# Kernel optimization log

Measured on AMD Instinct MI355X. Metric: run time of the kernel, lower is better.

## Reference

```python
import jax, jax.numpy as jnp
import numpy as np

EPS = 1e-7       # torchvision generalized_box_iou_loss eps
IMG_SIZE = 320.0  # labels are divided by 320 in the original criterion
NO_OBJ = 80       # class id 80 == no-object sentinel


def _hungarian(cost):
    """Jonker-Volgenant style shortest-augmenting-path LSA (== scipy.optimize.linear_sum_assignment).
    cost: [n, m] numpy array, n <= m. Returns (row_ind, col_ind) sorted by row."""
    cost = np.asarray(cost, dtype=np.float64)
    n, m = cost.shape
    INF = float("inf")
    u = np.zeros(n + 1)
    v = np.zeros(m + 1)
    p = np.zeros(m + 1, dtype=np.int64)   # p[j]: 1-based row matched to column j, 0 = free
    way = np.zeros(m + 1, dtype=np.int64)
    for i in range(1, n + 1):
        p[0] = i
        j0 = 0
        minv = np.full(m + 1, INF)
        used = np.zeros(m + 1, dtype=bool)
        while True:
            used[j0] = True
            i0 = p[j0]
            free = ~used[1:]
            cur = cost[i0 - 1] - u[i0] - v[1:]
            better = free & (cur < minv[1:])
            minv[1:] = np.where(better, cur, minv[1:])
            way[1:] = np.where(better, j0, way[1:])
            masked = np.where(free, minv[1:], INF)
            j1 = int(np.argmin(masked)) + 1
            delta = masked[j1 - 1]
            uj = np.nonzero(used)[0]
            u[p[uj]] += delta
            v[uj] -= delta
            minv[1:] = np.where(free, minv[1:] - delta, minv[1:])
            j0 = j1
            if p[j0] == 0:
                break
        while j0 != 0:
            j1 = way[j0]
            p[j0] = p[j1]
            j0 = j1
    cols = np.nonzero(p[1:])[0]
    rows = p[1:][cols] - 1
    order = np.argsort(rows)
    return rows[order], cols[order]


def _box_cxcywh_to_xyxy(b):
    cx, cy, w, h = b[..., 0], b[..., 1], b[..., 2], b[..., 3]
    return jnp.stack([cx - 0.5 * w, cy - 0.5 * h, cx + 0.5 * w, cy + 0.5 * h], axis=-1)


def _cost_matrix(prob_class, predict_bbox, labels):
    """Vectorized version of the original nested double loop: [B, n_pred, n_true] cost."""
    B, P, C = prob_class.shape
    T = labels.shape[1]
    lab_bbox = labels[..., :4] / IMG_SIZE          # [B,T,4] cxcywh in [0,1]
    cls = labels[..., 4].astype(jnp.int32)          # [B,T]

    # class NLL: -log p[b, pred, cls[b, true]]
    logp = jnp.log(prob_class)                      # [B,P,C]
    idx = jnp.broadcast_to(cls[:, None, :], (B, P, T))
    class_nll = -jnp.take_along_axis(logp, idx, axis=2)   # [B,P,T]

    # pairwise L1 (mean over the 4 box coords)
    pb = predict_bbox[:, :, None, :]                # [B,P,1,4]
    lb = lab_bbox[:, None, :, :]                    # [B,1,T,4]
    l1 = jnp.abs(pb - lb).mean(axis=-1)             # [B,P,T]

    # pairwise GIoU loss (1 - GIoU), torchvision convention
    xp = _box_cxcywh_to_xyxy(predict_bbox)[:, :, None, :]   # [B,P,1,4]
    xl = _box_cxcywh_to_xyxy(lab_bbox)[:, None, :, :]       # [B,1,T,4]
    lt = jnp.maximum(xp[..., :2], xl[..., :2])
    rb = jnp.minimum(xp[..., 2:], xl[..., 2:])
    wh = jnp.clip(rb - lt, 0.0)
    inter = wh[..., 0] * wh[..., 1]                          # [B,P,T]
    area_p = (xp[..., 2] - xp[..., 0]) * (xp[..., 3] - xp[..., 1])
    area_l = (xl[..., 2] - xl[..., 0]) * (xl[..., 3] - xl[..., 1])
    union = area_p + area_l - inter
    iou = inter / (union + EPS)
    ltc = jnp.minimum(xp[..., :2], xl[..., :2])
    rbc = jnp.maximum(xp[..., 2:], xl[..., 2:])
    whc = jnp.clip(rbc - ltc, 0.0)
    enclose = whc[..., 0] * whc[..., 1]
    giou = iou - (enclose - union) / (enclose + EPS)
    giou_loss = 1.0 - giou                                   # [B,P,T]

    no_obj_mask = (cls != NO_OBJ).astype(prob_class.dtype)[:, None, :]  # [B,1,T]
    return class_nll + (5.0 * l1 + 2.0 * giou_loss) * no_obj_mask


def setup_inputs() -> dict:
    key = jax.random.key(0)
    k1, k2, k3, k4 = jax.random.split(key, 4)
    B, P, T, C = 64, 150, 150, 81
    prob_class = jax.nn.softmax(jax.random.normal(k1, (B, P, C), jnp.float32), axis=-1)
    predict_bbox = jax.nn.sigmoid(jax.random.normal(k2, (B, P, 4), jnp.float32))
    lab_bbox = jax.random.uniform(k3, (B, T, 4), jnp.float32, 0.05, 0.95) * IMG_SIZE
    lab_cls = jax.random.randint(k4, (B, T), 0, 81).astype(jnp.float32)
    labels = jnp.concatenate([lab_bbox, lab_cls[..., None]], axis=-1)
    return {"prob_class": prob_class, "predict_bbox": predict_bbox, "labels": labels}


def reference(prob_class, predict_bbox, labels):
    cost = _cost_matrix(prob_class, predict_bbox, labels)   # [B,P,T]
    cost_np = np.asarray(cost)
    loss = jnp.zeros((), dtype=cost.dtype)
    for i in range(cost_np.shape[0]):
        r, c = _hungarian(cost_np[i])
        # faithful to the original (it indexes all batch elements with batch-i's matching)
        loss = loss + cost[:, r, c].mean()
    return loss
```

## Files before the change

### kernel.cpp

```cpp
#include <hip/hip_runtime.h>
#include <hip/hip_bf16.h>
#include <math.h>

#define B_   64
#define P_   150
#define T_   150
#define C_   81
#define NOOBJ 80

__global__ void cost_kernel(const float* __restrict__ prob,
                            const float* __restrict__ pbox,
                            const float* __restrict__ labels,
                            float* __restrict__ cost) {
    int idx = blockIdx.x * blockDim.x + threadIdx.x;
    const int total = B_ * P_ * T_;
    if (idx >= total) return;
    int t  = idx % T_;
    int p  = (idx / T_) % P_;
    int b  = idx / (P_ * T_);

    const float* lb5 = labels + ((size_t)b * T_ + t) * 5;
    const float inv = 1.0f / 320.0f;
    float lcx = lb5[0] * inv, lcy = lb5[1] * inv, lw = lb5[2] * inv, lh = lb5[3] * inv;
    int cls = (int)lb5[4];

    const float* pb = pbox + ((size_t)b * P_ + p) * 4;
    float pcx = pb[0], pcy = pb[1], pw = pb[2], ph = pb[3];

    float nll = -logf(prob[((size_t)b * P_ + p) * C_ + cls]);

    float l1 = 0.25f * (fabsf(pcx - lcx) + fabsf(pcy - lcy) +
                        fabsf(pw - lw)   + fabsf(ph - lh));

    float px0 = pcx - 0.5f * pw, py0 = pcy - 0.5f * ph;
    float px1 = pcx + 0.5f * pw, py1 = pcy + 0.5f * ph;
    float lx0 = lcx - 0.5f * lw, ly0 = lcy - 0.5f * lh;
    float lx1 = lcx + 0.5f * lw, ly1 = lcy + 0.5f * lh;

    float ltx = fmaxf(px0, lx0), lty = fmaxf(py0, ly0);
    float rbx = fminf(px1, lx1), rby = fminf(py1, ly1);
    float iw = fmaxf(rbx - ltx, 0.f), ih = fmaxf(rby - lty, 0.f);
    float inter = iw * ih;
    float ap = (px1 - px0) * (py1 - py0);
    float al = (lx1 - lx0) * (ly1 - ly0);
    float un = ap + al - inter;
    float iou = inter / (un + 1e-7f);

    float cx0 = fminf(px0, lx0), cy0 = fminf(py0, ly0);
    float cx1 = fmaxf(px1, lx1), cy1 = fmaxf(py1, ly1);
    float cw = fmaxf(cx1 - cx0, 0.f), ch = fmaxf(cy1 - cy0, 0.f);
    float enc = cw * ch;
    float giou = iou - (enc - un) / (enc + 1e-7f);
    float gl = 1.0f - giou;

    float mask = (cls != NOOBJ) ? 1.0f : 0.0f;
    cost[idx] = nll + (5.0f * l1 + 2.0f * gl) * mask;
}

#define SM_U      (P_ * T_ * 4)
#define SM_TOTAL  (SM_U + 152 * 8)

__device__ __forceinline__ unsigned ord32(float f) {
    unsigned bits = __float_as_uint(f);
    return (bits & 0x80000000u) ? ~bits : (bits | 0x80000000u);
}

#define DPPMIN(x, ctrl)                                                          \
    do {                                                                         \
        unsigned _t = (unsigned)__builtin_amdgcn_update_dpp(                     \
            (int)(x), (int)(x), (ctrl), 0xF, 0xF, false);                        \
        (x) = (_t < (x)) ? _t : (x);                                             \
    } while (0)

__device__ __forceinline__ int sel3i(int s, int a, int b, int c) {
    return s == 0 ? a : (s == 1 ? b : c);
}

__global__ __launch_bounds__(64) void hungarian_kernel(const float* __restrict__ cost,
                                                       int* __restrict__ assign) {
    const int b = blockIdx.x;
    const int lane = threadIdx.x;
    const float* Cg = cost + (size_t)b * (P_ * T_);

    extern __shared__ char smem[];
    float*  cl = (float*)smem;
    double* u  = (double*)(smem + SM_U);

    for (int i4 = lane; i4 < (P_ * T_) / 4; i4 += 64)
        ((float4*)cl)[i4] = ((const float4*)Cg)[i4];
    for (int r = lane; r <= P_; r += 64) u[r] = 0.0;
    __syncthreads();

    const int ja = 1 + lane;
    const int jb = 65 + lane;
    const int jc = 129 + lane;
    const bool va2 = (jc <= T_);
    const int jcs = va2 ? jc : T_;

    float m0 = cl[ja - 1], m1 = cl[jb - 1], m2 = cl[jcs - 1];
    #pragma unroll 4
    for (int r = 1; r < P_; ++r) {
        int rb_ = r * T_;
        m0 = fminf(m0, cl[rb_ + ja - 1]);
        m1 = fminf(m1, cl[rb_ + jb - 1]);
        m2 = fminf(m2, cl[rb_ + jcs - 1]);
    }
    double v0 = (double)m0, v1 = (double)m1, v2 = va2 ? (double)m2 : 0.0;
    int pa = 0, pb = 0, pc = 0;

    const double INF = __builtin_inf();

    for (int i = 1; i <= P_; ++i) {
        double mv0 = INF, mv1 = INF, mv2 = INF;
        int w0 = 0, w1 = 0, w2 = 0;
        int um = va2 ? 0 : 4;
        double ua = 0.0, ub = 0.0, uc = 0.0;
        int ra = 0, rb = 0, rc = 0;
        int j0 = 0;
        int i0cur = i;

        double ui0 = u[i];
        double u_i = ui0;
        int base = (i - 1) * T_ - 1;
        float c0 = cl[base + ja];
        float c1 = cl[base + jb];
        float c2 = cl[base + jcs];

        while (true) {
            if (j0 > 0 && lane == ((j0 - 1) & 63)) {
                int sl = (j0 - 1) >> 6;
                if (sl == 0)      { um |= 1; ua = ui0; ra = i0cur; }
                else if (sl == 1) { um |= 2; ub = ui0; rb = i0cur; }
                else              { um |= 4; uc = ui0; rc = i0cur; }
            }

            double cur0 = ((double)c0 - ui0) - v0;
            double cur1 = ((double)c1 - ui0) - v1;
            double cur2 = ((double)c2 - ui0) - v2;
            if (!(um & 1) && cur0 < mv0) { mv0 = cur0; w0 = j0; }
            if (!(um & 2) && cur1 < mv1) { mv1 = cur1; w1 = j0; }
            if (!(um & 4) && cur2 < mv2) { mv2 = cur2; w2 = j0; }

            double bestv = INF; int bestj = 0x7FFFFFFF; int bestp = 0;
            if (!(um & 1))                { bestv = mv0; bestj = ja; bestp = pa; }
            if (!(um & 2) && mv1 < bestv) { bestv = mv1; bestj = jb; bestp = pb; }
            if (!(um & 4) && mv2 < bestv) { bestv = mv2; bestj = jc; bestp = pc; }

            float kf = (float)bestv + 0.0f;
            unsigned key = ord32(kf);
            unsigned x = key;
            DPPMIN(x, 0x111);
            DPPMIN(x, 0x112);
            DPPMIN(x, 0x114);
            DPPMIN(x, 0x118);
            DPPMIN(x, 0x142);
            DPPMIN(x, 0x143);
            unsigned kmin = (unsigned)__builtin_amdgcn_readlane((int)x, 63);

            unsigned long long cm = __ballot(key == kmin);
            int j1, pj; double delta;
            int pk = (bestp << 8) | (bestj & 0xFF);
            if (__popcll(cm) == 1) {
                int L = (int)__builtin_ctzll(cm);
                int pkw = __builtin_amdgcn_readlane(pk, L);
                j1 = pkw & 0xFF;
                pj = pkw >> 8;
                int hi = __builtin_amdgcn_readlane(__double2hiint(bestv), L);
                int lo = __builtin_amdgcn_readlane(__double2loint(bestv), L);
                delta = __hiloint2double(hi, lo);
            } else {
                double bv = INF; int bj = 0x7FFFFFFF; int bp = 0;
                unsigned long long m = cm;
                while (m) {
                    int L = (int)__builtin_ctzll(m); m &= m - 1;
                    int hi = __builtin_amdgcn_readlane(__double2hiint(bestv), L);
                    int lo = __builtin_amdgcn_readlane(__double2loint(bestv), L);
                    double dv = __hiloint2double(hi, lo);
                    int dj = __builtin_amdgcn_readlane(bestj, L);
                    int dp = __builtin_amdgcn_readlane(bestp, L);
                    if (dv < bv || (dv == bv && dj < bj)) { bv = dv; bj = dj; bp = dp; }
                }
                j1 = bj; pj = bp; delta = bv;
            }

            int pr = (pj > 0) ? pj : 1;
            double ui_n = u[pr];
            int bn = (pr - 1) * T_ - 1;
            float c0n = cl[bn + ja];
            float c1n = cl[bn + jb];
            float c2n = cl[bn + jcs];

            if (um & 1) { v0 -= delta; ua += delta; } else { mv0 -= delta; }
            if (um & 2) { v1 -= delta; ub += delta; } else { mv1 -= delta; }
            if (va2) {
                if (um & 4) { v2 -= delta; uc += delta; } else { mv2 -= delta; }
            }
            u_i += delta;

            i0cur = pj;
            j0 = j1;
            if (pj == 0) break;
            ui0 = ui_n; c0 = c0n; c1 = c1n; c2 = c2n;
        }

        if (um & 1) u[ra] = ua;
        if (um & 2) u[rb] = ub;
        if (va2 && (um & 4)) u[rc] = uc;
        if (lane == 0) u[i] = u_i;

        int jj = j0;
        while (jj != 0) {
            int sj = (jj - 1) >> 6, lj = (jj - 1) & 63;
            int jn = __shfl(sel3i(sj, w0, w1, w2), lj);
            int rown;
            if (jn == 0) rown = i;
            else {
                int sn = (jn - 1) >> 6, ln = (jn - 1) & 63;
                rown = __shfl(sel3i(sn, pa, pb, pc), ln);
            }
            if (lane == lj) {
                if (sj == 0) pa = rown; else if (sj == 1) pb = rown; else pc = rown;
            }
            jj = jn;
        }
    }

    assign[b * P_ + (pa - 1)] = ja - 1;
    assign[b * P_ + (pb - 1)] = jb - 1;
    if (va2) assign[b * P_ + (pc - 1)] = jc - 1;
}

__global__ void gather_kernel(const float* __restrict__ cost,
                              const int* __restrict__ assign,
                              double* __restrict__ partial) {
    const int i = blockIdx.x;
    const int* a = assign + i * P_;
    double s = 0.0;
    for (int idx = threadIdx.x; idx < B_ * P_; idx += blockDim.x) {
        int b = idx / P_;
        int k = idx % P_;
        s += (double)cost[((size_t)b * P_ + k) * T_ + a[k]];
    }
    __shared__ double red[256];
    red[threadIdx.x] = s;
    __syncthreads();
    for (int off = 128; off >= 1; off >>= 1) {
        if (threadIdx.x < off) red[threadIdx.x] += red[threadIdx.x + off];
        __syncthreads();
    }
    if (threadIdx.x == 0) partial[i] = red[0] / (double)(B_ * P_);
}

__global__ void finalize_kernel(const double* __restrict__ partial,
                                float* __restrict__ out) {
    if (threadIdx.x == 0 && blockIdx.x == 0) {
        double s = 0.0;
        for (int i = 0; i < B_; ++i) s += partial[i];
        out[0] = (float)s;
    }
}

extern "C" void kernel_launch(void* const* d_in, const int* in_sizes, int n_in,
                              void* d_out, int out_size, void* d_ws, size_t ws_size,
                              hipStream_t stream) {
    const float* prob   = (const float*)d_in[0];
    const float* pbox   = (const float*)d_in[1];
    const float* labels = (const float*)d_in[2];
    float* out = (float*)d_out;

    char* ws = (char*)d_ws;
    float*  cost    = (float*) ws;
    int*    assign  = (int*)   (ws + (size_t)B_ * P_ * T_ * 4);
    double* partial = (double*)(ws + (size_t)B_ * P_ * T_ * 4 + (size_t)B_ * P_ * 4);

    const int total = B_ * P_ * T_;
    cost_kernel<<<(total + 255) / 256, 256, 0, stream>>>(prob, pbox, labels, cost);

    hungarian_kernel<<<B_, 64, SM_TOTAL, stream>>>(cost, assign);

    gather_kernel<<<B_, 256, 0, stream>>>(cost, assign, partial);

    finalize_kernel<<<1, 64, 0, stream>>>(partial, out);
}
```

Before: 1.240 ms.

## Add JV column-reduction and augmenting row-reduction warm start before Hungarian augmentation

Adds the Jonker-Volgenant initialization phases: column reduction records the argmin row per column and greedily assigns unique rows, then two passes of augmenting row reduction use the two smallest reduced costs per row to assign free rows cheaply. The main shortest-augmenting-path loop then skips rows that are already assigned. The aim is to cut the number of expensive Dijkstra-style augmentations done by the single wave, at the cost of extra serial readlane/ballot work and a risk of not reproducing scipy's exact tie-breaking assignment.

```diff
diff --git a/kernel.cpp b/kernel.cpp
--- a/kernel.cpp
+++ b/kernel.cpp
@@ -76,6 +76,36 @@
     return s == 0 ? a : (s == 1 ? b : c);
 }
 
+__device__ __forceinline__ void wave_argmin(double lval, int lpay,
+                                            double* oval, int* opay) {
+    float kf = (float)lval + 0.0f;
+    unsigned key = ord32(kf);
+    unsigned x = key;
+    DPPMIN(x, 0x111); DPPMIN(x, 0x112); DPPMIN(x, 0x114);
+    DPPMIN(x, 0x118); DPPMIN(x, 0x142); DPPMIN(x, 0x143);
+    unsigned kmin = (unsigned)__builtin_amdgcn_readlane((int)x, 63);
+    unsigned long long cm = __ballot(key == kmin);
+    if (__popcll(cm) == 1) {
+        int L = (int)__builtin_ctzll(cm);
+        int hi = __builtin_amdgcn_readlane(__double2hiint(lval), L);
+        int lo = __builtin_amdgcn_readlane(__double2loint(lval), L);
+        *oval = __hiloint2double(hi, lo);
+        *opay = __builtin_amdgcn_readlane(lpay, L);
+    } else {
+        double bv = __builtin_inf(); int bp = 0x7FFFFFFF;
+        unsigned long long m = cm;
+        while (m) {
+            int L = (int)__builtin_ctzll(m); m &= m - 1;
+            int hi = __builtin_amdgcn_readlane(__double2hiint(lval), L);
+            int lo = __builtin_amdgcn_readlane(__double2loint(lval), L);
+            double dv = __hiloint2double(hi, lo);
+            int dp = __builtin_amdgcn_readlane(lpay, L);
+            if (dv < bv || (dv == bv && dp < bp)) { bv = dv; bp = dp; }
+        }
+        *oval = bv; *opay = bp;
+    }
+}
+
 __global__ __launch_bounds__(64) void hungarian_kernel(const float* __restrict__ cost,
                                                        int* __restrict__ assign) {
     const int b = blockIdx.x;
@@ -97,20 +127,100 @@
     const bool va2 = (jc <= T_);
     const int jcs = va2 ? jc : T_;
 
+    const double INF = __builtin_inf();
+
     float m0 = cl[ja - 1], m1 = cl[jb - 1], m2 = cl[jcs - 1];
+    int i1a = 1, i1b = 1, i1c = 1;
     #pragma unroll 4
-    for (int r = 1; r < P_; ++r) {
-        int rb_ = r * T_;
-        m0 = fminf(m0, cl[rb_ + ja - 1]);
-        m1 = fminf(m1, cl[rb_ + jb - 1]);
-        m2 = fminf(m2, cl[rb_ + jcs - 1]);
+    for (int r = 2; r <= P_; ++r) {
+        int rb_ = (r - 1) * T_;
+        float t0 = cl[rb_ + ja - 1], t1 = cl[rb_ + jb - 1], t2 = cl[rb_ + jcs - 1];
+        if (t0 < m0) { m0 = t0; i1a = r; }
+        if (t1 < m1) { m1 = t1; i1b = r; }
+        if (t2 < m2) { m2 = t2; i1c = r; }
     }
     double v0 = (double)m0, v1 = (double)m1, v2 = va2 ? (double)m2 : 0.0;
     int pa = 0, pb = 0, pc = 0;
 
-    const double INF = __builtin_inf();
+    int frm = (lane < 22) ? 7 : 3;
+
+    for (int j = 1; j <= T_; ++j) {
+        int sl = (j - 1) >> 6, ol = (j - 1) & 63;
+        int i1 = __builtin_amdgcn_readlane(sel3i(sl, i1a, i1b, i1c), ol);
+        int rl = (i1 - 1) & 63, rs = (i1 - 1) >> 6;
+        int fm = __builtin_amdgcn_readlane(frm, rl);
+        if (fm & (1 << rs)) {
+            if (lane == ol) {
+                if (sl == 0) pa = i1; else if (sl == 1) pb = i1; else pc = i1;
+            }
+            if (lane == rl) frm &= ~(1 << rs);
+        }
+    }
+
+    for (int pass = 0; pass < 2; ++pass) {
+        for (int irow = 1; irow <= P_; ++irow) {
+            {
+                int rl = (irow - 1) & 63, rs = (irow - 1) >> 6;
+                int fm = __builtin_amdgcn_readlane(frm, rl);
+                if (!(fm & (1 << rs))) continue;
+            }
+            int i = irow;
+            for (int guard = 0; guard < 256; ++guard) {
+                int base = (i - 1) * T_ - 1;
+                float f0 = cl[base + ja], f1 = cl[base + jb], f2 = cl[base + jcs];
+                double r0 = (double)f0 - v0;
+                double r1 = (double)f1 - v1;
+                double r2 = va2 ? ((double)f2 - v2) : INF;
+                double lm1, lm2; int lj1, lj2;
+                if (r0 <= r1) { lm1 = r0; lj1 = ja; lm2 = r1; lj2 = jb; }
+                else          { lm1 = r1; lj1 = jb; lm2 = r0; lj2 = ja; }
+                if (r2 < lm1)      { lm2 = lm1; lj2 = lj1; lm1 = r2; lj1 = jc; }
+                else if (r2 < lm2) { lm2 = r2; lj2 = jc; }
+
+                double umin; int j1;
+                wave_argmin(lm1, lj1, &umin, &j1);
+                double s1 = (lj1 == j1) ? lm2 : lm1;
+                int    sj = (lj1 == j1) ? lj2 : lj1;
+                double usub; int j2;
+                wave_argmin(s1, sj, &usub, &j2);
+
+                bool strict = (umin < usub);
+                int jt = j1;
+                if (strict) {
+                    double d = usub - umin;
+                    if (lane == ((j1 - 1) & 63)) {
+                        int sl = (j1 - 1) >> 6;
+                        if (sl == 0) v0 -= d; else if (sl == 1) v1 -= d; else v2 -= d;
+                    }
+                } else {
+                    int sl = (j1 - 1) >> 6, ol = (j1 - 1) & 63;
+                    int pj1 = __builtin_amdgcn_readlane(sel3i(sl, pa, pb, pc), ol);
+                    if (pj1 != 0) jt = j2;
+                }
+                int slt = (jt - 1) >> 6, olt = (jt - 1) & 63;
+                int k = __builtin_amdgcn_readlane(sel3i(slt, pa, pb, pc), olt);
+                if (lane == olt) {
+                    if (slt == 0) pa = i; else if (slt == 1) pb = i; else pc = i;
+                }
+                if (lane == 0) u[i] = strict ? usub : umin;
+                { int rl = (i - 1) & 63, rs = (i - 1) >> 6;
+                  if (lane == rl) frm &= ~(1 << rs); }
+                if (k != 0) {
+                    int rl = (k - 1) & 63, rs = (k - 1) >> 6;
+                    if (lane == rl) frm |= (1 << rs);
+                }
+                if (k == 0 || !strict) break;
+                i = k;
+            }
+        }
+    }
 
     for (int i = 1; i <= P_; ++i) {
+        {
+            int rl = (i - 1) & 63, rs = (i - 1) >> 6;
+            int fm = __builtin_amdgcn_readlane(frm, rl);
+            if (!(fm & (1 << rs))) continue;
+        }
         double mv0 = INF, mv1 = INF, mv2 = INF;
         int w0 = 0, w1 = 0, w2 = 0;
         int um = va2 ? 0 : 4;
@@ -149,12 +259,8 @@
             float kf = (float)bestv + 0.0f;
             unsigned key = ord32(kf);
             unsigned x = key;
-            DPPMIN(x, 0x111);
-            DPPMIN(x, 0x112);
-            DPPMIN(x, 0x114);
-            DPPMIN(x, 0x118);
-            DPPMIN(x, 0x142);
-            DPPMIN(x, 0x143);
+            DPPMIN(x, 0x111); DPPMIN(x, 0x112); DPPMIN(x, 0x114);
+            DPPMIN(x, 0x118); DPPMIN(x, 0x142); DPPMIN(x, 0x143);
             unsigned kmin = (unsigned)__builtin_amdgcn_readlane((int)x, 63);
 
             unsigned long long cm = __ballot(key == kmin);
```

Result: slower. 2.065 ms (+66.6%).
